# Kernel tuning notes

Measured on AMD Instinct MI355X. Metric: run time of the kernel, lower is better.

The kernel has to match this reference:

```python
import jax, jax.numpy as jnp
import numpy as np

# Inner recurrent cell: u' = BETA*u + x @ W ; out s = tanh(u')
# diag-RTRL trace: E' = du_du * E + du_dp = BETA * E + x[:, :, None]
BETA = 0.9
B, D_IN, D_H = 32, 1024, 1024


def setup_inputs() -> dict:
    key = jax.random.key(0)
    k1, k2, k3 = jax.random.split(key, 3)
    x = jax.random.normal(k1, (B, D_IN), dtype=jnp.float32)
    W = jax.random.normal(k2, (D_IN, D_H), dtype=jnp.float32) / np.sqrt(D_IN).astype(np.float32)
    u = jax.random.normal(k3, (B, D_H), dtype=jnp.float32)
    E = jnp.zeros((B, D_IN, D_H), dtype=jnp.float32)  # eligibility trace, zeros at init (as in __init__)
    return {"x": x, "W": W, "u": u, "E": E}


def reference(x, W, u, E):
    # forward of the wrapped model, vmapped over batch (here fully vectorized)
    u_new = BETA * u + x @ W          # [B, D_H] new recurrent state
    s = jnp.tanh(u_new)               # [B, D_H] output
    # Jacobian diagonals (what jacrev(sum_output) computes analytically):
    #   du_du = BETA (const),  du_dp[b,i,j] = x[b,i]
    # diag_rtrl_update: E' = du_du * E + du_dp
    E_new = BETA * E + x[:, :, None]  # [B, D_IN, D_H]
    # Return output, updated state, updated trace (module stores u_new/E_new as side effects)
    return s, u_new, E_new
```

## Files before the change

### kernel.cpp

```cpp
#include <hip/hip_runtime.h>
#include <math.h>


#define BETA 0.9f

constexpr int Bb   = 32;
constexpr int D_IN = 1024;
constexpr int D_H  = 1024;

constexpr int THREADS    = 256;
constexpr int KSPLIT     = 32;
constexpr int JTILES     = 16;
constexpr int GEMM_TILES = KSPLIT * JTILES;
constexpr int GRID1      = 2048;
constexpr int TRIPS_G    = 13;
constexpr int TRIPS_E    = 17;

typedef float f4 __attribute__((ext_vector_type(4)));

__global__ __launch_bounds__(THREADS) void rtrl_k1(
    const float* __restrict__ x,
    const float* __restrict__ W,
    const float* __restrict__ E,
    float* __restrict__ out,
    float* __restrict__ ws)
{
    __shared__ float Wt[32][64];
    __shared__ float xs[32][32];

    const int blk = blockIdx.x;
    const int tid = threadIdx.x;

    if (blk < GEMM_TILES) {
        const int kt = blk >> 4;
        const int jt = blk & 15;
        const int i0 = kt * 32;
        const int j0 = jt * 64;

        const f4* __restrict__ W4 = (const f4*)W;
        const f4* __restrict__ x4 = (const f4*)x;

        {
            f4* Wt4 = (f4*)Wt;
            #pragma unroll
            for (int p = 0; p < 2; ++p) {
                const int idx = tid + p * 256;
                const int row = idx >> 4, c4 = idx & 15;
                Wt4[row * 16 + c4] = W4[(i0 + row) * 256 + (j0 >> 2) + c4];
            }
        }
        {
            f4* xs4 = (f4*)xs;
            const int row = tid >> 3, c4 = tid & 7;
            xs4[row * 8 + c4] = x4[row * 256 + (i0 >> 2) + c4];
        }
        __syncthreads();

        const int bg = tid >> 6;
        const int jc = tid & 63;
        float a0=0,a1=0,a2=0,a3=0,a4=0,a5=0,a6=0,a7=0;
        #pragma unroll 8
        for (int i = 0; i < 32; ++i) {
            const float wv = Wt[i][jc];
            a0 = fmaf(xs[bg*8+0][i], wv, a0);
            a1 = fmaf(xs[bg*8+1][i], wv, a1);
            a2 = fmaf(xs[bg*8+2][i], wv, a2);
            a3 = fmaf(xs[bg*8+3][i], wv, a3);
            a4 = fmaf(xs[bg*8+4][i], wv, a4);
            a5 = fmaf(xs[bg*8+5][i], wv, a5);
            a6 = fmaf(xs[bg*8+6][i], wv, a6);
            a7 = fmaf(xs[bg*8+7][i], wv, a7);
        }
        float acc[8] = {a0,a1,a2,a3,a4,a5,a6,a7};
        #pragma unroll
        for (int bb = 0; bb < 8; ++bb) {
            const int b = bg * 8 + bb;
            ws[(kt * Bb + b) * D_H + j0 + jc] = acc[bb];
        }
    }

    const f4* __restrict__ E4 = (const f4*)E;
    f4* __restrict__ O4 = (f4*)(out + 2 * Bb * D_H);

    const int ntrips = (blk < GEMM_TILES) ? TRIPS_G : TRIPS_E;
    const int r0     = (blk < GEMM_TILES)
                     ? blk * (TRIPS_G * THREADS)
                     : GEMM_TILES * (TRIPS_G * THREADS) + (blk - GEMM_TILES) * (TRIPS_E * THREADS);

    int v = r0 + tid;
    int t = 0;
    for (; t + 4 <= ntrips; t += 4) {
        f4 e0 = E4[v];
        f4 e1 = E4[v + 256];
        f4 e2 = E4[v + 512];
        f4 e3 = E4[v + 768];
        const float x0 = x[v >> 8];
        const float x1 = x[(v + 256) >> 8];
        const float x2 = x[(v + 512) >> 8];
        const float x3 = x[(v + 768) >> 8];
        __builtin_nontemporal_store(e0 * BETA + x0, &O4[v]);
        __builtin_nontemporal_store(e1 * BETA + x1, &O4[v + 256]);
        __builtin_nontemporal_store(e2 * BETA + x2, &O4[v + 512]);
        __builtin_nontemporal_store(e3 * BETA + x3, &O4[v + 768]);
        v += 1024;
    }
    for (; t < ntrips; ++t) {
        f4 e = E4[v];
        const float xv = x[v >> 8];
        __builtin_nontemporal_store(e * BETA + xv, &O4[v]);
        v += 256;
    }
}

__global__ __launch_bounds__(THREADS) void rtrl_k2(
    const float* __restrict__ ws,
    const float* __restrict__ u,
    float* __restrict__ out)
{
    const int t = blockIdx.x * THREADS + threadIdx.x;
    float acc = 0.f;
    #pragma unroll
    for (int k = 0; k < KSPLIT; ++k)
        acc += ws[k * (Bb * D_H) + t];
    const float un = BETA * u[t] + acc;
    out[t]            = tanhf(un);
    out[Bb * D_H + t] = un;
}

extern "C" void kernel_launch(void* const* d_in, const int* in_sizes, int n_in,
                              void* d_out, int out_size, void* d_ws, size_t ws_size,
                              hipStream_t stream) {
    const float* x = (const float*)d_in[0];
    const float* W = (const float*)d_in[1];
    const float* u = (const float*)d_in[2];
    const float* E = (const float*)d_in[3];
    float* out = (float*)d_out;
    float* ws  = (float*)d_ws;

    rtrl_k1<<<GRID1, THREADS, 0, stream>>>(x, W, E, out, ws);
    rtrl_k2<<<(Bb * D_H) / THREADS, THREADS, 0, stream>>>(ws, u, out);
}
```

Baseline: 48.57 us.

## Fuse split-K reduction into main kernel via atomic completion counter

Replaces the second reduction kernel with a tail stage in the last 128 blocks of the main kernel. Those blocks spin on a global atomic counter until all GEMM tiles have written their partial sums, then reduce them and apply tanh. This removes one kernel launch and its boundary, but adds a hipMemsetAsync before the launch. It also relies on the GEMM blocks being scheduled before the waiting blocks, otherwise the spin-wait could deadlock.

```diff
diff --git a/kernel.cpp b/kernel.cpp
--- a/kernel.cpp
+++ b/kernel.cpp
@@ -15,15 +15,20 @@
 constexpr int GRID1      = 2048;
 constexpr int TRIPS_G    = 13;
 constexpr int TRIPS_E    = 17;
+constexpr int RED_BLOCKS = 128;
+constexpr size_t PART_BYTES = (size_t)KSPLIT * Bb * D_H * sizeof(float);
 
 typedef float f4 __attribute__((ext_vector_type(4)));
 
+template <bool FUSED>
 __global__ __launch_bounds__(THREADS) void rtrl_k1(
     const float* __restrict__ x,
     const float* __restrict__ W,
+    const float* __restrict__ u,
     const float* __restrict__ E,
     float* __restrict__ out,
-    float* __restrict__ ws)
+    float* __restrict__ ws,
+    unsigned* __restrict__ cnt)
 {
     __shared__ float Wt[32][64];
     __shared__ float xs[32][32];
@@ -77,38 +82,66 @@
             const int b = bg * 8 + bb;
             ws[(kt * Bb + b) * D_H + j0 + jc] = acc[bb];
         }
+
+        if (FUSED) {
+            __syncthreads();
+            if (tid == 0) {
+                __threadfence();
+                atomicAdd(cnt, 1u);
+            }
+        }
     }
 
-    const f4* __restrict__ E4 = (const f4*)E;
-    f4* __restrict__ O4 = (f4*)(out + 2 * Bb * D_H);
+    {
+        const f4* __restrict__ E4 = (const f4*)E;
+        f4* __restrict__ O4 = (f4*)(out + 2 * Bb * D_H);
 
-    const int ntrips = (blk < GEMM_TILES) ? TRIPS_G : TRIPS_E;
-    const int r0     = (blk < GEMM_TILES)
-                     ? blk * (TRIPS_G * THREADS)
-                     : GEMM_TILES * (TRIPS_G * THREADS) + (blk - GEMM_TILES) * (TRIPS_E * THREADS);
+        const int ntrips = (blk < GEMM_TILES) ? TRIPS_G : TRIPS_E;
+        const int r0     = (blk < GEMM_TILES)
+                         ? blk * (TRIPS_G * THREADS)
+                         : GEMM_TILES * (TRIPS_G * THREADS) + (blk - GEMM_TILES) * (TRIPS_E * THREADS);
 
-    int v = r0 + tid;
-    int t = 0;
-    for (; t + 4 <= ntrips; t += 4) {
-        f4 e0 = E4[v];
-        f4 e1 = E4[v + 256];
-        f4 e2 = E4[v + 512];
-        f4 e3 = E4[v + 768];
-        const float x0 = x[v >> 8];
-        const float x1 = x[(v + 256) >> 8];
-        const float x2 = x[(v + 512) >> 8];
-        const float x3 = x[(v + 768) >> 8];
-        __builtin_nontemporal_store(e0 * BETA + x0, &O4[v]);
-        __builtin_nontemporal_store(e1 * BETA + x1, &O4[v + 256]);
-        __builtin_nontemporal_store(e2 * BETA + x2, &O4[v + 512]);
-        __builtin_nontemporal_store(e3 * BETA + x3, &O4[v + 768]);
-        v += 1024;
+        int v = r0 + tid;
+        int t = 0;
+        for (; t + 4 <= ntrips; t += 4) {
+            f4 e0 = E4[v];
+            f4 e1 = E4[v + 256];
+            f4 e2 = E4[v + 512];
+            f4 e3 = E4[v + 768];
+            const float x0 = x[v >> 8];
+            const float x1 = x[(v + 256) >> 8];
+            const float x2 = x[(v + 512) >> 8];
+            const float x3 = x[(v + 768) >> 8];
+            __builtin_nontemporal_store(e0 * BETA + x0, &O4[v]);
+            __builtin_nontemporal_store(e1 * BETA + x1, &O4[v + 256]);
+            __builtin_nontemporal_store(e2 * BETA + x2, &O4[v + 512]);
+            __builtin_nontemporal_store(e3 * BETA + x3, &O4[v + 768]);
+            v += 1024;
+        }
+        for (; t < ntrips; ++t) {
+            f4 e = E4[v];
+            const float xv = x[v >> 8];
+            __builtin_nontemporal_store(e * BETA + xv, &O4[v]);
+            v += 256;
+        }
     }
-    for (; t < ntrips; ++t) {
-        f4 e = E4[v];
-        const float xv = x[v >> 8];
-        __builtin_nontemporal_store(e * BETA + xv, &O4[v]);
-        v += 256;
+
+    if (FUSED && blk >= GRID1 - RED_BLOCKS) {
+        if (tid == 0) {
+            while (atomicAdd(cnt, 0u) < (unsigned)GEMM_TILES)
+                __builtin_amdgcn_s_sleep(8);
+        }
+        __syncthreads();
+        __threadfence();
+
+        const int t = (blk - (GRID1 - RED_BLOCKS)) * THREADS + tid;
+        float acc = 0.f;
+        #pragma unroll
+        for (int k = 0; k < KSPLIT; ++k)
+            acc += ws[k * (Bb * D_H) + t];
+        const float un = BETA * u[t] + acc;
+        out[t]            = tanhf(un);
+        out[Bb * D_H + t] = un;
     }
 }
 
@@ -137,6 +170,12 @@
     float* out = (float*)d_out;
     float* ws  = (float*)d_ws;
 
-    rtrl_k1<<<GRID1, THREADS, 0, stream>>>(x, W, E, out, ws);
-    rtrl_k2<<<(Bb * D_H) / THREADS, THREADS, 0, stream>>>(ws, u, out);
+    if (ws_size >= PART_BYTES + sizeof(unsigned)) {
+        unsigned* cnt = (unsigned*)((char*)d_ws + PART_BYTES);
+        hipMemsetAsync(cnt, 0, sizeof(unsigned), stream);
+        rtrl_k1<true><<<GRID1, THREADS, 0, stream>>>(x, W, u, E, out, ws, cnt);
+    } else {
+        rtrl_k1<false><<<GRID1, THREADS, 0, stream>>>(x, W, u, E, out, ws, nullptr);
+        rtrl_k2<<<(Bb * D_H) / THREADS, THREADS, 0, stream>>>(ws, u, out);
+    }
 }
```

Result: slower. 83.47 us (+71.8%).
